# Kernel tuning notes

Hardware: AMD Instinct MI355X
Metric: run time of the kernel (lower is better)

Reference implementation:

```python
import jax, jax.numpy as jnp
import numpy as np

B, S, H = 32, 2048, 1024


def setup_inputs() -> dict:
    key = jax.random.key(0)
    k1, k2, k3, k4, k5 = jax.random.split(key, 5)
    # scale linear weights like torch default init (~U(-1/sqrt(fan_in),..)); normal*small is fine for a numeric baseline
    return {
        "hidden": jax.random.normal(k1, (B, H), dtype=jnp.float32),
        "encoder_outputs": jax.random.normal(k2, (B, S, H), dtype=jnp.float32),
        "attn_w": jax.random.normal(k3, (H, 2 * H), dtype=jnp.float32) * (1.0 / np.sqrt(2 * H)),
        "attn_b": jax.random.normal(k4, (H,), dtype=jnp.float32) * (1.0 / np.sqrt(2 * H)),
        "v_w": jax.random.normal(k5, (1, H), dtype=jnp.float32) * (1.0 / np.sqrt(H)),
    }


def reference(hidden, encoder_outputs, attn_w, attn_b, v_w):
    # hidden: [B,H]; encoder_outputs: [B,S,H]
    # torch: cat((hidden repeated over S, enc), dim=2) @ attn_w.T + attn_b
    # Split attn_w columns: first H cols act on hidden, last H cols on enc.
    # Avoids materializing the repeated/concatenated [B,S,2H] tensor.
    Hdim = hidden.shape[-1]
    Wh = attn_w[:, :Hdim]   # [H, H] applied to hidden
    We = attn_w[:, Hdim:]   # [H, H] applied to encoder outputs
    # [B,1,H] + [B,S,H] + [H] -> tanh -> [B,S,H]
    e = jnp.tanh((hidden @ Wh.T)[:, None, :] + jnp.einsum('bsh,kh->bsk', encoder_outputs, We) + attn_b)
    scores = jnp.einsum('bsh,h->bs', e, v_w[0])          # [B,S], v has no bias
    attn_weights = jax.nn.softmax(scores, axis=1)        # softmax over source positions (dim=1)
    context = jnp.einsum('bs,bsh->bh', attn_weights, encoder_outputs)  # [B,H]
    output = jnp.concatenate([context, hidden], axis=1)  # [B,2H]
    return output, attn_weights[..., None]               # match torch shapes: [B,2H], [B,S,1]
```

## Files before the change

### kernel.cpp

```cpp
#include <hip/hip_runtime.h>
#include <stdint.h>

#define BATCH 32
#define SEQ   2048
#define HDIM  1024

typedef short short8 __attribute__((ext_vector_type(8)));
typedef float f32x4 __attribute__((ext_vector_type(4)));

__device__ __forceinline__ unsigned short f2b(float f) {
    unsigned u = __float_as_uint(f);
    u += 0x7FFFu + ((u >> 16) & 1u);
    return (unsigned short)(u >> 16);
}
__device__ __forceinline__ unsigned pk_bf16(float a, float b) {
    return __builtin_amdgcn_perm(__float_as_uint(b), __float_as_uint(a), 0x07060302u);
}
__device__ __forceinline__ float fast_tanh(float x) {
    float ex = __expf(2.0f * x);
    return 1.0f - 2.0f / (ex + 1.0f);
}
__device__ __forceinline__ void gl2lds16(const unsigned short* g, unsigned short* l) {
    __builtin_amdgcn_global_load_lds(
        (const __attribute__((address_space(1))) unsigned int*)g,
        (__attribute__((address_space(3))) unsigned int*)l, 16, 0, 0);
}

__global__ __launch_bounds__(256) void prep_kernel(
    const float* __restrict__ hidden, const float* __restrict__ attn_w,
    const float* __restrict__ attn_b, unsigned short* __restrict__ we_bf,
    float* __restrict__ qb, float* __restrict__ scores) {
    int k = blockIdx.x;
    int tid = threadIdx.x;

    if (tid < 64) scores[(size_t)k * 64 + tid] = 0.0f;

    {
        const float4* src = (const float4*)(attn_w + (size_t)k * 2048 + 1024);
        float4 v = src[tid];
        ushort4 o;
        o.x = f2b(v.x); o.y = f2b(v.y); o.z = f2b(v.z); o.w = f2b(v.w);
        ((ushort4*)(we_bf + (size_t)k * HDIM))[tid] = o;
    }

    float part[BATCH];
#pragma unroll
    for (int b = 0; b < BATCH; ++b) part[b] = 0.0f;
    const float* wrow = attn_w + (size_t)k * 2048;
    for (int h = tid; h < HDIM; h += 256) {
        float w = wrow[h];
#pragma unroll
        for (int b = 0; b < BATCH; ++b) part[b] += w * hidden[b * HDIM + h];
    }
    __shared__ float red[4][BATCH];
    int lane = tid & 63, wv = tid >> 6;
#pragma unroll
    for (int b = 0; b < BATCH; ++b) {
        float v = part[b];
        v += __shfl_xor(v, 1);  v += __shfl_xor(v, 2);  v += __shfl_xor(v, 4);
        v += __shfl_xor(v, 8);  v += __shfl_xor(v, 16); v += __shfl_xor(v, 32);
        if (lane == 0) red[wv][b] = v;
    }
    __syncthreads();
    if (tid < BATCH) {
        float v = red[0][tid] + red[1][tid] + red[2][tid] + red[3][tid] + attn_b[k];
        qb[(size_t)tid * HDIM + k] = v;
    }
}

__global__ __launch_bounds__(512, 2) void score_gemm_kernel(
    const float* __restrict__ enc, const unsigned short* __restrict__ we_bf,
    const float* __restrict__ qb, const float* __restrict__ v_w,
    float* __restrict__ scores) {
    __shared__ __align__(16) unsigned short As[2 * 8192];
    __shared__ __align__(16) unsigned short Bs[2 * 8192];

    int tid  = threadIdx.x;
    int lane = tid & 63, w = tid >> 6;
    int wm = w & 1, wn = w >> 1;
    int i15 = lane & 15, q = lane >> 4;

    int raw   = blockIdx.x;
    int ntile = (raw >> 3) & 3;
    int mtile = (raw & 7) + 8 * (raw >> 5);
    int n0 = ntile * 256;
    long gm0 = (long)mtile * 256;
    int b = mtile >> 3;

    int brow_in = lane >> 2;
    int bchunk  = (lane & 3) ^ ((lane >> 3) & 3);
    const unsigned short* Bg =
        we_bf + (size_t)(n0 + w * 16 + brow_in) * HDIM + bchunk * 8;

    int ra = tid >> 1, h = tid & 1;
    const float* Ag = enc + (size_t)(gm0 + ra) * HDIM + h * 16;
    int swz = (ra >> 1) & 3;
    int p0 = (2 * h) ^ swz, p1 = (2 * h + 1) ^ swz;

    f32x4 acc[8][4];
#pragma unroll
    for (int mt = 0; mt < 8; ++mt)
#pragma unroll
        for (int nt = 0; nt < 4; ++nt) acc[mt][nt] = (f32x4)0.0f;

    int xoff = (q ^ ((i15 >> 1) & 3)) * 8;
    int arow0 = wm * 128 + i15;
    int brow0 = wn * 64 + i15;

    float4 pre[4];

#define STAGE(KT, BUF) do {                                                   \
        unsigned short* bd = Bs + (BUF) * 8192 + (w * 16) * 32 + lane * 8;    \
        const unsigned short* bsrc = Bg + (size_t)(KT) * 32;                  \
        gl2lds16(bsrc, bd);                                                   \
        gl2lds16(bsrc + (size_t)128 * HDIM, bd + 128 * 32);                   \
        const float4* ap = (const float4*)(Ag + (size_t)(KT) * 32);           \
        pre[0] = ap[0]; pre[1] = ap[1]; pre[2] = ap[2]; pre[3] = ap[3];       \
    } while (0)

#define DSW(BUF) do {                                                         \
        unsigned short* ad = As + (BUF) * 8192 + ra * 32;                     \
        uint4 u0, u1;                                                         \
        u0.x = pk_bf16(pre[0].x, pre[0].y); u0.y = pk_bf16(pre[0].z, pre[0].w);\
        u0.z = pk_bf16(pre[1].x, pre[1].y); u0.w = pk_bf16(pre[1].z, pre[1].w);\
        u1.x = pk_bf16(pre[2].x, pre[2].y); u1.y = pk_bf16(pre[2].z, pre[2].w);\
        u1.z = pk_bf16(pre[3].x, pre[3].y); u1.w = pk_bf16(pre[3].z, pre[3].w);\
        *(uint4*)(ad + p0 * 8) = u0;                                          \
        *(uint4*)(ad + p1 * 8) = u1;                                          \
    } while (0)

    STAGE(0, 0);
    DSW(0);
    __syncthreads();

#pragma unroll 2
    for (int kt = 0; kt < 32; ++kt) {
        int cur = kt & 1;
        if (kt < 31) STAGE(kt + 1, cur ^ 1);

        const unsigned short* Ac = As + cur * 8192;
        const unsigned short* Bc = Bs + cur * 8192;

        short8 bf[4];
#pragma unroll
        for (int nt = 0; nt < 4; ++nt)
            bf[nt] = *(const short8*)(Bc + (brow0 + nt * 16) * 32 + xoff);

        __builtin_amdgcn_s_setprio(1);
#pragma unroll
        for (int mt = 0; mt < 8; ++mt) {
            short8 af = *(const short8*)(Ac + (arow0 + mt * 16) * 32 + xoff);
#pragma unroll
            for (int nt = 0; nt < 4; ++nt)
                acc[mt][nt] = __builtin_amdgcn_mfma_f32_16x16x32_bf16(
                    af, bf[nt], acc[mt][nt], 0, 0, 0);
        }
        __builtin_amdgcn_s_setprio(0);

        if (kt < 31) {
            DSW(cur ^ 1);
            __syncthreads();
        }
    }
#undef STAGE
#undef DSW

    float sc[8][4];
#pragma unroll
    for (int mt = 0; mt < 8; ++mt)
#pragma unroll
        for (int r = 0; r < 4; ++r) sc[mt][r] = 0.0f;

#pragma unroll
    for (int nt = 0; nt < 4; ++nt) {
        int n = n0 + wn * 64 + nt * 16 + i15;
        float qv = qb[(size_t)b * HDIM + n];
        float vv = v_w[n];
#pragma unroll
        for (int mt = 0; mt < 8; ++mt)
#pragma unroll
            for (int r = 0; r < 4; ++r)
                sc[mt][r] += vv * fast_tanh(acc[mt][nt][r] + qv);
    }
#pragma unroll
    for (int mt = 0; mt < 8; ++mt)
#pragma unroll
        for (int r = 0; r < 4; ++r) {
            float v = sc[mt][r];
            v += __shfl_xor(v, 1); v += __shfl_xor(v, 2);
            v += __shfl_xor(v, 4); v += __shfl_xor(v, 8);
            if (i15 == 0)
                atomicAdd(&scores[gm0 + wm * 128 + mt * 16 + q * 4 + r], v);
        }
}

__global__ __launch_bounds__(256) void softmax_kernel(
    const float* __restrict__ scores, const float* __restrict__ hidden,
    float* out) {
    int b = blockIdx.x, tid = threadIdx.x;
    const float* srow = scores + (size_t)b * SEQ;
    __shared__ float redm[4];
    __shared__ float reds[4];
    int lane = tid & 63, wv = tid >> 6;

    float loc[8];
    float m = -1e30f;
#pragma unroll
    for (int i = 0; i < 8; ++i) {
        loc[i] = srow[tid + i * 256];
        m = fmaxf(m, loc[i]);
    }
#pragma unroll
    for (int d = 1; d < 64; d <<= 1) m = fmaxf(m, __shfl_xor(m, d));
    if (lane == 0) redm[wv] = m;
    __syncthreads();
    m = fmaxf(fmaxf(redm[0], redm[1]), fmaxf(redm[2], redm[3]));

    float sum = 0.0f;
#pragma unroll
    for (int i = 0; i < 8; ++i) {
        float e = __expf(loc[i] - m);
        loc[i] = e;
        sum += e;
    }
#pragma unroll
    for (int d = 1; d < 64; d <<= 1) sum += __shfl_xor(sum, d);
    if (lane == 0) reds[wv] = sum;
    __syncthreads();
    sum = reds[0] + reds[1] + reds[2] + reds[3];
    float inv = 1.0f / sum;

#pragma unroll
    for (int i = 0; i < 8; ++i)
        out[BATCH * SEQ + (size_t)b * SEQ + tid + i * 256] = loc[i] * inv;

    for (int i = tid; i < HDIM; i += 256) {
        out[(size_t)b * 2048 + i] = 0.0f;
        out[(size_t)b * 2048 + 1024 + i] = hidden[(size_t)b * HDIM + i];
    }
}

__global__ __launch_bounds__(256) void context_kernel(
    const float* __restrict__ enc, const float* __restrict__ weights_src,
    float* out) {
    int id = blockIdx.x;
    int scid = id & 31, b = id >> 5;
    int tid = threadIdx.x;
    __shared__ float wl[64];
    if (tid < 64)
        wl[tid] = weights_src[BATCH * SEQ + (size_t)b * SEQ + scid * 64 + tid];
    __syncthreads();
    const float* ebase = enc + ((size_t)(b * SEQ + scid * 64)) * HDIM + tid * 4;
    float a0 = 0.f, a1 = 0.f, a2 = 0.f, a3 = 0.f;
#pragma unroll 8
    for (int s = 0; s < 64; ++s) {
        float4 e = *(const float4*)(ebase + (size_t)s * HDIM);
        float w = wl[s];
        a0 += w * e.x; a1 += w * e.y; a2 += w * e.z; a3 += w * e.w;
    }
    float* o = out + (size_t)b * 2048 + tid * 4;
    atomicAdd(o + 0, a0); atomicAdd(o + 1, a1);
    atomicAdd(o + 2, a2); atomicAdd(o + 3, a3);
}

extern "C" void kernel_launch(void* const* d_in, const int* in_sizes, int n_in,
                              void* d_out, int out_size, void* d_ws, size_t ws_size,
                              hipStream_t stream) {
    const float* hidden = (const float*)d_in[0];
    const float* enc    = (const float*)d_in[1];
    const float* attn_w = (const float*)d_in[2];
    const float* attn_b = (const float*)d_in[3];
    const float* v_w    = (const float*)d_in[4];
    float* out = (float*)d_out;

    char* ws = (char*)d_ws;
    unsigned short* we_bf = (unsigned short*)ws;
    float* qb     = (float*)(ws + (size_t)2097152);
    float* scores = (float*)(ws + (size_t)2097152 + 131072);

    prep_kernel<<<1024, 256, 0, stream>>>(hidden, attn_w, attn_b, we_bf, qb, scores);
    score_gemm_kernel<<<1024, 512, 0, stream>>>(enc, we_bf, qb, v_w, scores);
    softmax_kernel<<<32, 256, 0, stream>>>(scores, hidden, out);
    context_kernel<<<1024, 256, 0, stream>>>(enc, out, out);
}
```

Measured before the change: 635.1 us.

## Retile score GEMM to 128x128 tiles with K-step 64 and widen context blocks

Changes the score GEMM from 256x256 tiles with 512 threads to 128x128 tiles with 256 threads and a K-step of 64, using a new XOR swizzle and 4096 blocks. The context kernel processes 128 sequence rows per block with two independent accumulator streams, halving its atomic count. Smaller tiles give more parallelism and lower register pressure, but increase redundant reads and bf16 conversion of the fp32 encoder outputs.

After: 722.3 us. 1.14x slower.

```diff
diff --git a/kernel.cpp b/kernel.cpp
--- a/kernel.cpp
+++ b/kernel.cpp
@@ -68,7 +68,7 @@
     }
 }
 
-__global__ __launch_bounds__(512, 2) void score_gemm_kernel(
+__global__ __launch_bounds__(256, 2) void score_gemm_kernel(
     const float* __restrict__ enc, const unsigned short* __restrict__ we_bf,
     const float* __restrict__ qb, const float* __restrict__ v_w,
     float* __restrict__ scores) {
@@ -81,52 +81,55 @@
     int i15 = lane & 15, q = lane >> 4;
 
     int raw   = blockIdx.x;
-    int ntile = (raw >> 3) & 3;
-    int mtile = (raw & 7) + 8 * (raw >> 5);
-    int n0 = ntile * 256;
-    long gm0 = (long)mtile * 256;
-    int b = mtile >> 3;
-
-    int brow_in = lane >> 2;
-    int bchunk  = (lane & 3) ^ ((lane >> 3) & 3);
+    int ntile = (raw >> 3) & 7;
+    int mtile = (raw & 7) + 8 * (raw >> 6);
+    int n0 = ntile * 128;
+    long gm0 = (long)mtile * 128;
+    int b = mtile >> 4;
+
+    int brow_in = lane >> 3;
+    int bchunk  = (lane & 7) ^ ((lane >> 3) & 7);
     const unsigned short* Bg =
-        we_bf + (size_t)(n0 + w * 16 + brow_in) * HDIM + bchunk * 8;
+        we_bf + (size_t)(n0 + w * 32 + brow_in) * HDIM + bchunk * 8;
+    unsigned short* Bw_dst_base;
 
     int ra = tid >> 1, h = tid & 1;
-    const float* Ag = enc + (size_t)(gm0 + ra) * HDIM + h * 16;
-    int swz = (ra >> 1) & 3;
-    int p0 = (2 * h) ^ swz, p1 = (2 * h + 1) ^ swz;
-
-    f32x4 acc[8][4];
-#pragma unroll
-    for (int mt = 0; mt < 8; ++mt)
+    const float* Ag = enc + (size_t)(gm0 + ra) * HDIM + h * 32;
+    int aswz = ra & 7;
+
+    f32x4 acc[4][4];
+#pragma unroll
+    for (int mt = 0; mt < 4; ++mt)
 #pragma unroll
         for (int nt = 0; nt < 4; ++nt) acc[mt][nt] = (f32x4)0.0f;
 
-    int xoff = (q ^ ((i15 >> 1) & 3)) * 8;
-    int arow0 = wm * 128 + i15;
+    int arow0 = wm * 64 + i15;
     int brow0 = wn * 64 + i15;
 
-    float4 pre[4];
+    float4 pre[8];
 
 #define STAGE(KT, BUF) do {                                                   \
-        unsigned short* bd = Bs + (BUF) * 8192 + (w * 16) * 32 + lane * 8;    \
-        const unsigned short* bsrc = Bg + (size_t)(KT) * 32;                  \
-        gl2lds16(bsrc, bd);                                                   \
-        gl2lds16(bsrc + (size_t)128 * HDIM, bd + 128 * 32);                   \
-        const float4* ap = (const float4*)(Ag + (size_t)(KT) * 32);           \
+        unsigned short* bd = Bs + (BUF) * 8192 + (w * 32) * 64 + lane * 8;    \
+        const unsigned short* bsrc = Bg + (size_t)(KT) * 64;                  \
+        gl2lds16(bsrc,                        bd);                            \
+        gl2lds16(bsrc + (size_t)8  * HDIM,    bd + 512);                      \
+        gl2lds16(bsrc + (size_t)16 * HDIM,    bd + 1024);                     \
+        gl2lds16(bsrc + (size_t)24 * HDIM,    bd + 1536);                     \
+        const float4* ap = (const float4*)(Ag + (size_t)(KT) * 64);           \
         pre[0] = ap[0]; pre[1] = ap[1]; pre[2] = ap[2]; pre[3] = ap[3];       \
+        pre[4] = ap[4]; pre[5] = ap[5]; pre[6] = ap[6]; pre[7] = ap[7];       \
     } while (0)
 
 #define DSW(BUF) do {                                                         \
-        unsigned short* ad = As + (BUF) * 8192 + ra * 32;                     \
-        uint4 u0, u1;                                                         \
-        u0.x = pk_bf16(pre[0].x, pre[0].y); u0.y = pk_bf16(pre[0].z, pre[0].w);\
-        u0.z = pk_bf16(pre[1].x, pre[1].y); u0.w = pk_bf16(pre[1].z, pre[1].w);\
-        u1.x = pk_bf16(pre[2].x, pre[2].y); u1.y = pk_bf16(pre[2].z, pre[2].w);\
-        u1.z = pk_bf16(pre[3].x, pre[3].y); u1.w = pk_bf16(pre[3].z, pre[3].w);\
-        *(uint4*)(ad + p0 * 8) = u0;                                          \
-        *(uint4*)(ad + p1 * 8) = u1;                                          \
+        unsigned short* ad = As + (BUF) * 8192 + ra * 64;                     \
+        _Pragma("unroll")                                                     \
+        for (int j = 0; j < 4; ++j) {                                         \
+            float4 x = pre[2 * j], y = pre[2 * j + 1];                        \
+            uint4 o;                                                          \
+            o.x = pk_bf16(x.x, x.y); o.y = pk_bf16(x.z, x.w);                 \
+            o.z = pk_bf16(y.x, y.y); o.w = pk_bf16(y.z, y.w);                 \
+            *(uint4*)(ad + ((4 * h + j) ^ aswz) * 8) = o;                     \
+        }                                                                     \
     } while (0)
 
     STAGE(0, 0);
@@ -134,30 +137,34 @@
     __syncthreads();
 
 #pragma unroll 2
-    for (int kt = 0; kt < 32; ++kt) {
+    for (int kt = 0; kt < 16; ++kt) {
         int cur = kt & 1;
-        if (kt < 31) STAGE(kt + 1, cur ^ 1);
+        if (kt < 15) STAGE(kt + 1, cur ^ 1);
 
         const unsigned short* Ac = As + cur * 8192;
         const unsigned short* Bc = Bs + cur * 8192;
 
-        short8 bf[4];
-#pragma unroll
-        for (int nt = 0; nt < 4; ++nt)
-            bf[nt] = *(const short8*)(Bc + (brow0 + nt * 16) * 32 + xoff);
-
         __builtin_amdgcn_s_setprio(1);
 #pragma unroll
-        for (int mt = 0; mt < 8; ++mt) {
-            short8 af = *(const short8*)(Ac + (arow0 + mt * 16) * 32 + xoff);
+        for (int kk = 0; kk < 2; ++kk) {
+            int xr = ((kk * 4 + q) ^ (i15 & 7)) * 8;
+            short8 af[4], bf[4];
+#pragma unroll
+            for (int mt = 0; mt < 4; ++mt)
+                af[mt] = *(const short8*)(Ac + (arow0 + mt * 16) * 64 + xr);
 #pragma unroll
             for (int nt = 0; nt < 4; ++nt)
-                acc[mt][nt] = __builtin_amdgcn_mfma_f32_16x16x32_bf16(
-                    af, bf[nt], acc[mt][nt], 0, 0, 0);
+                bf[nt] = *(const short8*)(Bc + (brow0 + nt * 16) * 64 + xr);
+#pragma unroll
+            for (int mt = 0; mt < 4; ++mt)
+#pragma unroll
+                for (int nt = 0; nt < 4; ++nt)
+                    acc[mt][nt] = __builtin_amdgcn_mfma_f32_16x16x32_bf16(
+                        af[mt], bf[nt], acc[mt][nt], 0, 0, 0);
         }
         __builtin_amdgcn_s_setprio(0);
 
-        if (kt < 31) {
+        if (kt < 15) {
             DSW(cur ^ 1);
             __syncthreads();
         }
@@ -165,9 +172,9 @@
 #undef STAGE
 #undef DSW
 
-    float sc[8][4];
-#pragma unroll
-    for (int mt = 0; mt < 8; ++mt)
+    float sc[4][4];
+#pragma unroll
+    for (int mt = 0; mt < 4; ++mt)
 #pragma unroll
         for (int r = 0; r < 4; ++r) sc[mt][r] = 0.0f;
 
@@ -177,20 +184,20 @@
         float qv = qb[(size_t)b * HDIM + n];
         float vv = v_w[n];
 #pragma unroll
-        for (int mt = 0; mt < 8; ++mt)
+        for (int mt = 0; mt < 4; ++mt)
 #pragma unroll
             for (int r = 0; r < 4; ++r)
                 sc[mt][r] += vv * fast_tanh(acc[mt][nt][r] + qv);
     }
 #pragma unroll
-    for (int mt = 0; mt < 8; ++mt)
+    for (int mt = 0; mt < 4; ++mt)
 #pragma unroll
         for (int r = 0; r < 4; ++r) {
             float v = sc[mt][r];
             v += __shfl_xor(v, 1); v += __shfl_xor(v, 2);
             v += __shfl_xor(v, 4); v += __shfl_xor(v, 8);
             if (i15 == 0)
-                atomicAdd(&scores[gm0 + wm * 128 + mt * 16 + q * 4 + r], v);
+                atomicAdd(&scores[gm0 + wm * 64 + mt * 16 + q * 4 + r], v);
         }
 }
 
@@ -244,23 +251,26 @@
     const float* __restrict__ enc, const float* __restrict__ weights_src,
     float* out) {
     int id = blockIdx.x;
-    int scid = id & 31, b = id >> 5;
+    int scid = id & 15, b = id >> 4;
     int tid = threadIdx.x;
-    __shared__ float wl[64];
-    if (tid < 64)
-        wl[tid] = weights_src[BATCH * SEQ + (size_t)b * SEQ + scid * 64 + tid];
-    __syncthreads();
-    const float* ebase = enc + ((size_t)(b * SEQ + scid * 64)) * HDIM + tid * 4;
+    __shared__ float wl[128];
+    if (tid < 128)
+        wl[tid] = weights_src[BATCH * SEQ + (size_t)b * SEQ + scid * 128 + tid];
+    __syncthreads();
+    const float* ebase = enc + ((size_t)(b * SEQ + scid * 128)) * HDIM + tid * 4;
     float a0 = 0.f, a1 = 0.f, a2 = 0.f, a3 = 0.f;
-#pragma unroll 8
+    float b0 = 0.f, b1 = 0.f, b2 = 0.f, b3 = 0.f;
+#pragma unroll 4
     for (int s = 0; s < 64; ++s) {
-        float4 e = *(const float4*)(ebase + (size_t)s * HDIM);
-        float w = wl[s];
-        a0 += w * e.x; a1 += w * e.y; a2 += w * e.z; a3 += w * e.w;
+        float4 e0 = *(const float4*)(ebase + (size_t)s * HDIM);
+        float4 e1 = *(const float4*)(ebase + (size_t)(s + 64) * HDIM);
+        float w0 = wl[s], w1 = wl[s + 64];
+        a0 += w0 * e0.x; a1 += w0 * e0.y; a2 += w0 * e0.z; a3 += w0 * e0.w;
+        b0 += w1 * e1.x; b1 += w1 * e1.y; b2 += w1 * e1.z; b3 += w1 * e1.w;
     }
     float* o = out + (size_t)b * 2048 + tid * 4;
-    atomicAdd(o + 0, a0); atomicAdd(o + 1, a1);
-    atomicAdd(o + 2, a2); atomicAdd(o + 3, a3);
+    atomicAdd(o + 0, a0 + b0); atomicAdd(o + 1, a1 + b1);
+    atomicAdd(o + 2, a2 + b2); atomicAdd(o + 3, a3 + b3);
 }
 
 extern "C" void kernel_launch(void* const* d_in, const int* in_sizes, int n_in,
@@ -279,7 +289,7 @@
     float* scores = (float*)(ws + (size_t)2097152 + 131072);
 
     prep_kernel<<<1024, 256, 0, stream>>>(hidden, attn_w, attn_b, we_bf, qb, scores);
-    score_gemm_kernel<<<1024, 512, 0, stream>>>(enc, we_bf, qb, v_w, scores);
+    score_gemm_kernel<<<4096, 256, 0, stream>>>(enc, we_bf, qb, v_w, scores);
     softmax_kernel<<<32, 256, 0, stream>>>(scores, hidden, out);
-    context_kernel<<<1024, 256, 0, stream>>>(enc, out, out);
-}
+    context_kernel<<<512, 256, 0, stream>>>(enc, out, out);
+}
```
